# Performance work log

Hardware: AMD Instinct MI355X
Metric: run time of the kernel (lower is better)

Reference implementation:

```python
import jax, jax.numpy as jnp
import numpy as np

# Dimensions (TinyLlama-like)
B, T = 4, 1024
D = 2048          # hidden_size
H, DH = 32, 64    # heads, head_dim
HK = 8            # kv heads (GQA, n_rep = 4)
RQ, RKV = 32, 32  # per-head SVD ranks
RO, RF = 1024, 1024
I = 5632          # intermediate_size
THETA = 10000.0
EPS = 1e-5


def setup_inputs() -> dict:
    key = jax.random.key(0)
    ks = jax.random.split(key, 16)
    p = lambda k, s: jax.random.normal(k, s, jnp.float32) * 0.02
    return {
        "x": jax.random.normal(ks[0], (B, T, D), jnp.float32),
        "ln1_w": jnp.ones((D,), jnp.float32),
        "ln2_w": jnp.ones((D,), jnp.float32),
        "q_Us": p(ks[1], (H, DH, RQ)),  "q_V": p(ks[2], (H, RQ, D)),
        "k_Us": p(ks[3], (HK, DH, RKV)), "k_V": p(ks[4], (HK, RKV, D)),
        "v_Us": p(ks[5], (HK, DH, RKV)), "v_V": p(ks[6], (HK, RKV, D)),
        "o_Us": p(ks[7], (D, RO)),  "o_V": p(ks[8], (RO, H * DH)),
        "g_Us": p(ks[9], (I, RF)),  "g_V": p(ks[10], (RF, D)),
        "u_Us": p(ks[11], (I, RF)), "u_V": p(ks[12], (RF, D)),
        "d_Us": p(ks[13], (D, RF)), "d_V": p(ks[14], (RF, I)),
    }


def _rms(x, w):
    return x * jax.lax.rsqrt(jnp.mean(x * x, axis=-1, keepdims=True) + EPS) * w


def _rope_cos_sin(t_len, dh, dtype):
    half = dh // 2
    inv_freq = 1.0 / (THETA ** (jnp.arange(half, dtype=jnp.float32) / half))
    ang = jnp.arange(t_len, dtype=jnp.float32)[:, None] * inv_freq[None, :]  # [T, half]
    return jnp.cos(ang).astype(dtype), jnp.sin(ang).astype(dtype)


def _apply_rope(x, cos, sin):
    # x: [B,h,T,Dh], LLaMA half-split rotation
    half = x.shape[-1] // 2
    x1, x2 = x[..., :half], x[..., half:]
    c = cos[None, None]  # [1,1,T,half]
    s = sin[None, None]
    return jnp.concatenate([x1 * c - x2 * s, x2 * c + x1 * s], axis=-1)


def reference(x, ln1_w, ln2_w, q_Us, q_V, k_Us, k_V, v_Us, v_V,
              o_Us, o_V, g_Us, g_V, u_Us, u_V, d_Us, d_V):
    b, t, d = x.shape
    h1 = _rms(x, ln1_w)

    # per-head low-rank projections: y_h = x @ V_h^T @ Us_h^T
    q = jnp.einsum('bhtr,hdr->bhtd', jnp.einsum('btD,hrD->bhtr', h1, q_V), q_Us)  # [B,H,T,Dh]
    k = jnp.einsum('bhtr,hdr->bhtd', jnp.einsum('btD,hrD->bhtr', h1, k_V), k_Us)  # [B,Hk,T,Dh]
    v = jnp.einsum('bhtr,hdr->bhtd', jnp.einsum('btD,hrD->bhtr', h1, v_V), v_Us)

    cos, sin = _rope_cos_sin(t, DH, x.dtype)
    q = _apply_rope(q, cos, sin)
    k = _apply_rope(k, cos, sin)

    n_rep = H // HK
    k = jnp.repeat(k, n_rep, axis=1)  # _repeat_kv
    v = jnp.repeat(v, n_rep, axis=1)

    scale = 1.0 / np.sqrt(DH)
    scores = jnp.einsum('bhtd,bhsd->bhts', q, k) * scale
    causal = jnp.tril(jnp.ones((t, t), bool))
    scores = jnp.where(causal[None, None], scores, jnp.finfo(scores.dtype).min)
    attn = jax.nn.softmax(scores, axis=-1)
    ctx = jnp.einsum('bhts,bhsd->bhtd', attn, v)
    ctx = ctx.transpose(0, 2, 1, 3).reshape(b, t, H * DH)

    # low-rank output proj: o = ctx @ o_V^T @ o_Us^T
    attn_out = jnp.einsum('btr,Dr->btD', jnp.einsum('btk,rk->btr', ctx, o_V), o_Us)
    x = x + attn_out

    # SwiGLU MLP with low-rank factors
    h2 = _rms(x, ln2_w)
    g = jnp.einsum('btr,ir->bti', jnp.einsum('btD,rD->btr', h2, g_V), g_Us)
    u = jnp.einsum('btr,ir->bti', jnp.einsum('btD,rD->btr', h2, u_V), u_Us)
    ff = jax.nn.silu(g) * u
    down = jnp.einsum('btr,Dr->btD', jnp.einsum('bti,ri->btr', ff, d_V), d_Us)
    return x + down
```

## Files before the change

kernel.cpp:

```cpp
#include <hip/hip_runtime.h>
#include <math.h>

typedef unsigned short u16;
typedef unsigned int u32;
typedef __bf16 bf16x8 __attribute__((ext_vector_type(8)));
typedef float f32x4 __attribute__((ext_vector_type(4)));

__device__ __forceinline__ float bf2f(u16 u) {
  union { u32 i; float f; } x; x.i = ((u32)u) << 16; return x.f;
}
__device__ __forceinline__ u16 f2bf(float f) {
  union { float f; u32 i; } x; x.f = f;
  return (u16)((x.i + 0x7fffu + ((x.i >> 16) & 1u)) >> 16);
}

#define GLDS16(gp, lp)                                                        \
  __builtin_amdgcn_global_load_lds(                                           \
      (const __attribute__((address_space(1))) u32*)(gp),                     \
      (__attribute__((address_space(3))) u32*)(lp), 16, 0, 0)

__global__ void detect_k(const u16* __restrict__ w, int* __restrict__ flag) {
  if (threadIdx.x == 0 && blockIdx.x == 0)
    *flag = (w[0] == 0x0000u && w[1] == 0x3F80u) ? 1 : 0;
}

__global__ __launch_bounds__(256) void rope_tab_k(float2* __restrict__ tab) {
  const int idx = blockIdx.x * 256 + threadIdx.x;
  const int t = idx >> 5, j = idx & 31;
  float inv = powf(10000.0f, -(float)j * (1.0f / 32.0f));
  float ang = (float)t * inv;
  float sn, cs;
  sincosf(ang, &sn, &cs);
  tab[idx] = make_float2(cs, sn);
}

struct CvtArgs {
  const void* src[17];
  u32 dstOff[17];
  u32 blkOff[18];
};

__global__ __launch_bounds__(256) void cvt_all(CvtArgs a, u16* __restrict__ dstB,
                                               const int* __restrict__ flag,
                                               const void* __restrict__ w1src,
                                               u16* __restrict__ h1) {
  int seg = 0;
  const int bx = blockIdx.x;
#pragma unroll 1
  while (bx >= (int)a.blkOff[seg + 1]) seg++;
  const int tid = threadIdx.x;
  const long local = ((long)(bx - a.blkOff[seg]) * 256 + tid) * 8;
  u16* dst = dstB + a.dstOff[seg] + local;
  const bool f32in = (*flag != 0);
  uint4 o; u16* op = (u16*)&o;
  if (f32in) {
    const float* s = (const float*)a.src[seg] + local;
    float4 va = *(const float4*)(s);
    float4 vb = *(const float4*)(s + 4);
    op[0] = f2bf(va.x); op[1] = f2bf(va.y); op[2] = f2bf(va.z); op[3] = f2bf(va.w);
    op[4] = f2bf(vb.x); op[5] = f2bf(vb.y); op[6] = f2bf(vb.z); op[7] = f2bf(vb.w);
  } else {
    o = *(const uint4*)((const u16*)a.src[seg] + local);
  }
  *(uint4*)dst = o;

  if (seg == 0) {
    float v[8];
    float ss = 0.f;
#pragma unroll
    for (int i = 0; i < 8; i++) { v[i] = bf2f(op[i]); ss += v[i] * v[i]; }
#pragma unroll
    for (int off = 32; off > 0; off >>= 1) ss += __shfl_xor(ss, off);
    __shared__ float red[4];
    if ((tid & 63) == 0) red[tid >> 6] = ss;
    __syncthreads();
    const float total = red[0] + red[1] + red[2] + red[3];
    const float inv = rsqrtf(total * (1.0f / 2048.0f) + 1e-5f);
    float wv[8];
    if (f32in) {
      const float* wp = (const float*)w1src + tid * 8;
      float4 wa = *(const float4*)(wp);
      float4 wb = *(const float4*)(wp + 4);
      wv[0] = bf2f(f2bf(wa.x)); wv[1] = bf2f(f2bf(wa.y));
      wv[2] = bf2f(f2bf(wa.z)); wv[3] = bf2f(f2bf(wa.w));
      wv[4] = bf2f(f2bf(wb.x)); wv[5] = bf2f(f2bf(wb.y));
      wv[6] = bf2f(f2bf(wb.z)); wv[7] = bf2f(f2bf(wb.w));
    } else {
      uint4 ww = *((const uint4*)w1src + tid);
      const u16* wp = (const u16*)&ww;
#pragma unroll
      for (int i = 0; i < 8; i++) wv[i] = bf2f(wp[i]);
    }
    uint4 ho; u16* hop = (u16*)&ho;
#pragma unroll
    for (int i = 0; i < 8; i++) hop[i] = f2bf(v[i] * inv * wv[i]);
    *(uint4*)(h1 + (long)bx * 2048 + tid * 8) = ho;
  }
}

__global__ __launch_bounds__(256) void rms_k(const u16* __restrict__ x,
                                             const u16* __restrict__ w,
                                             u16* __restrict__ out) {
  const long row = blockIdx.x;
  const u16* xr = x + row * 2048;
  u16* orow = out + row * 2048;
  const int tid = threadIdx.x;
  const int base = tid * 8;
  uint4 u = *(const uint4*)(xr + base);
  const u16* us = (const u16*)&u;
  float v[8];
  float ss = 0.f;
#pragma unroll
  for (int i = 0; i < 8; i++) { v[i] = bf2f(us[i]); ss += v[i] * v[i]; }
#pragma unroll
  for (int off = 32; off > 0; off >>= 1) ss += __shfl_xor(ss, off);
  __shared__ float red[4];
  if ((tid & 63) == 0) red[tid >> 6] = ss;
  __syncthreads();
  float total = red[0] + red[1] + red[2] + red[3];
  float inv = rsqrtf(total * (1.0f / 2048.0f) + 1e-5f);
  uint4 wv = *(const uint4*)(w + base);
  const u16* wp = (const u16*)&wv;
  uint4 o;
  u16* op = (u16*)&o;
#pragma unroll
  for (int i = 0; i < 8; i++) op[i] = f2bf(v[i] * inv * bf2f(wp[i]));
  *(uint4*)(orow + base) = o;
}

template <int EPI>
__global__ __launch_bounds__(256, 3) void gemm_bt(const u16* __restrict__ A,
                                                  const u16* __restrict__ B,
                                                  void* Cv,
                                                  void* Cv2,
                                                  const u16* R,
                                                  const int* flagp,
                                                  int N, int Klen, int lda, int ldb) {
  __shared__ u16 As[128 * 32];
  __shared__ u16 Bs[128 * 32];
  const long koff = (long)blockIdx.z * Klen;
  A += koff;
  B += koff;
  if (blockIdx.z) Cv = Cv2;
  const int m0 = blockIdx.y * 128;
  const int n0 = blockIdx.x * 128;
  const int tid = threadIdx.x;
  const int wave = tid >> 6;
  const int lane = tid & 63;
  const int wr = (wave >> 1) * 64;
  const int wc = (wave & 1) * 64;
  const int l16 = lane & 15;
  const int quad = lane >> 4;
  u16* C = (u16*)Cv;
  float* Cf = (float*)Cv;
  bool f32o = false;
  if (EPI == 3) f32o = (*flagp != 0);

  f32x4 acc[4][4];
#pragma unroll
  for (int i = 0; i < 4; i++)
#pragma unroll
    for (int j = 0; j < 4; j++) acc[i][j] = (f32x4){0.f, 0.f, 0.f, 0.f};

  const int srow = wave * 16 + (lane >> 2);
  const int scol = (lane & 3) * 8;
  const u16* Ag = A + (long)(m0 + srow) * lda + scol;
  const u16* Bg = B + (long)(n0 + srow) * ldb + scol;
  const long astep = (long)64 * lda;
  const long bstep = (long)64 * ldb;
  u16* Asw = &As[wave * 16 * 32];
  u16* Bsw = &Bs[wave * 16 * 32];

  for (int k0 = 0; k0 < Klen; k0 += 32) {
    GLDS16(Ag + k0, Asw);
    GLDS16(Ag + astep + k0, Asw + 64 * 32);
    GLDS16(Bg + k0, Bsw);
    GLDS16(Bg + bstep + k0, Bsw + 64 * 32);
    __syncthreads();
    bf16x8 af[4], bfr[4];
#pragma unroll
    for (int t = 0; t < 4; t++) {
      af[t]  = *(const bf16x8*)(&As[(wr + t * 16 + l16) * 32 + quad * 8]);
      bfr[t] = *(const bf16x8*)(&Bs[(wc + t * 16 + l16) * 32 + quad * 8]);
    }
#pragma unroll
    for (int i = 0; i < 4; i++)
#pragma unroll
      for (int j = 0; j < 4; j++)
        acc[i][j] = __builtin_amdgcn_mfma_f32_16x16x32_bf16(bfr[j], af[i], acc[i][j], 0, 0, 0);
    __syncthreads();
  }

#pragma unroll
  for (int i = 0; i < 4; i++) {
    const int m = m0 + wr + i * 16 + l16;
#pragma unroll
    for (int j = 0; j < 4; j++) {
      const int n = n0 + wc + j * 16 + quad * 4;
      const long idx = (long)m * N + n;
      float v[4];
#pragma unroll
      for (int r = 0; r < 4; r++) v[r] = acc[i][j][r];
      if (EPI == 1 || EPI == 3) {
        uint2 rr = *(const uint2*)(R + idx);
        const u16* rp = (const u16*)&rr;
#pragma unroll
        for (int r = 0; r < 4; r++) v[r] += bf2f(rp[r]);
      }
      if (EPI == 3 && f32o) {
        float4 o = {v[0], v[1], v[2], v[3]};
        *(float4*)(Cf + idx) = o;
      } else {
        uint2 o; u16* op = (u16*)&o;
#pragma unroll
        for (int r = 0; r < 4; r++) op[r] = f2bf(v[r]);
        *(uint2*)(C + idx) = o;
      }
    }
  }
}

#define STAGE_SILU(buf, k0)                                                   \
  do {                                                                        \
    GLDS16(Ag_ + (k0), &SH[buf][0][woff]);                                    \
    GLDS16(Au_ + (k0), &SH[buf][1][woff]);                                    \
    GLDS16(Bg_ + (k0), &SH[buf][2][woff]);                                    \
    GLDS16(Bu_ + (k0), &SH[buf][3][woff]);                                    \
  } while (0)

__global__ __launch_bounds__(512, 4) void gemm_silu(const u16* __restrict__ Agp,
                                                    const u16* __restrict__ Aup,
                                                    const u16* __restrict__ Bgp,
                                                    const u16* __restrict__ Bup,
                                                    u16* __restrict__ C,
                                                    int N, int Klen, int lda, int ldb) {
  __shared__ u16 SH[2][4][128 * 32];
  const int m0 = blockIdx.y * 128;
  const int n0 = blockIdx.x * 128;
  const int tid = threadIdx.x;
  const int wave = tid >> 6;
  const int lane = tid & 63;
  const int wid = wave & 3;
  const int isU = wave >> 2;
  const int wr = (wid >> 1) * 64;
  const int wc = (wid & 1) * 64;
  const int l16 = lane & 15;
  const int quad = lane >> 4;
  const int matA = isU;
  const int matB = 2 + isU;

  f32x4 acc[4][4];
#pragma unroll
  for (int i = 0; i < 4; i++)
#pragma unroll
    for (int j = 0; j < 4; j++) acc[i][j] = (f32x4){0.f, 0.f, 0.f, 0.f};

  const int srow = wave * 16 + (lane >> 2);
  const int scol = ((lane & 3) ^ ((lane >> 3) & 3)) * 8;
  const u16* Ag_ = Agp + (long)(m0 + srow) * lda + scol;
  const u16* Au_ = Aup + (long)(m0 + srow) * lda + scol;
  const u16* Bg_ = Bgp + (long)(n0 + srow) * ldb + scol;
  const u16* Bu_ = Bup + (long)(n0 + srow) * ldb + scol;
  const int woff = wave * 512;
  const int rsw = (quad ^ ((l16 >> 1) & 3)) * 8;

  const int nk = Klen >> 5;
  STAGE_SILU(0, 0);
  int cur = 0;
  for (int kt = 0; kt < nk; ++kt) {
    if (kt + 1 < nk) {
      STAGE_SILU(cur ^ 1, (kt + 1) << 5);
      asm volatile("s_waitcnt vmcnt(4)" ::: "memory");
    } else {
      asm volatile("s_waitcnt vmcnt(0)" ::: "memory");
    }
    asm volatile("s_barrier" ::: "memory");
    bf16x8 af[4], bfr[4];
#pragma unroll
    for (int t = 0; t < 4; t++) {
      af[t]  = *(const bf16x8*)(&SH[cur][matA][(wr + t * 16 + l16) * 32 + rsw]);
      bfr[t] = *(const bf16x8*)(&SH[cur][matB][(wc + t * 16 + l16) * 32 + rsw]);
    }
#pragma unroll
    for (int i = 0; i < 4; i++)
#pragma unroll
      for (int j = 0; j < 4; j++)
        acc[i][j] = __builtin_amdgcn_mfma_f32_16x16x32_bf16(bfr[j], af[i], acc[i][j], 0, 0, 0);
    asm volatile("s_barrier" ::: "memory");
    cur ^= 1;
  }

  float* xch = (float*)&SH[0][0][0];
  if (isU) {
    float* w = xch + wid * 4096 + lane * 4;
#pragma unroll
    for (int i = 0; i < 4; i++)
#pragma unroll
      for (int j = 0; j < 4; j++)
        *(f32x4*)(w + (i * 4 + j) * 256) = acc[i][j];
  }
  __syncthreads();
  if (!isU) {
    const float* w = xch + wid * 4096 + lane * 4;
#pragma unroll
    for (int i = 0; i < 4; i++) {
      const int m = m0 + wr + i * 16 + l16;
#pragma unroll
      for (int j = 0; j < 4; j++) {
        const int n = n0 + wc + j * 16 + quad * 4;
        const long idx = (long)m * N + n;
        f32x4 uv = *(const f32x4*)(w + (i * 4 + j) * 256);
        uint2 o; u16* op = (u16*)&o;
#pragma unroll
        for (int r = 0; r < 4; r++) {
          float g = acc[i][j][r];
          float v = uv[r] * g / (1.f + __expf(-g));
          op[r] = f2bf(v);
        }
        *(uint2*)(C + idx) = o;
      }
    }
  }
}

__global__ __launch_bounds__(256) void combine2(const u16* __restrict__ a,
                                                const u16* __restrict__ b,
                                                u16* __restrict__ o) {
  const long i = ((long)blockIdx.x * 256 + threadIdx.x) * 8;
  uint4 ua = *(const uint4*)(a + i);
  uint4 ub = *(const uint4*)(b + i);
  const u16* pa = (const u16*)&ua;
  const u16* pb = (const u16*)&ub;
  uint4 uo; u16* po = (u16*)&uo;
#pragma unroll
  for (int j = 0; j < 8; j++) po[j] = f2bf(bf2f(pa[j]) + bf2f(pb[j]));
  *(uint4*)(o + i) = uo;
}

__global__ __launch_bounds__(256) void expand_fused(const u16* __restrict__ p0,
                                                    const u16* __restrict__ p1,
                                                    const u16* __restrict__ qUs,
                                                    const u16* __restrict__ kUs,
                                                    const u16* __restrict__ vUs,
                                                    u16* __restrict__ qout,
                                                    u16* __restrict__ kout,
                                                    u16* __restrict__ vout,
                                                    const float2* __restrict__ tab) {
  const int tok = blockIdx.x;
  const int wave = threadIdx.x >> 6;
  const int d = threadIdx.x & 63;
  const int y = blockIdx.y;
  int mode, hbase;
  if (y < 8)       { mode = 0; hbase = y * 4; }
  else if (y < 10) { mode = 1; hbase = (y - 8) * 4; }
  else             { mode = 2; hbase = (y - 10) * 4; }
  const int h = hbase + wave;
  const int b = tok >> 10;
  const int t = tok & 1023;
  const int roff = (mode == 0) ? 0 : (mode == 1 ? 1024 : 1280);
  const u16* Us = (mode == 0) ? qUs : (mode == 1 ? kUs : vUs);
  const u16* up = Us + ((long)h * 64 + d) * 32;
  const long rbase = (long)tok * 1536 + roff + h * 32;
  const u16* rp0 = p0 + rbase;
  const u16* rp1 = p1 + rbase;
  float s = 0.f;
#pragma unroll
  for (int c = 0; c < 4; c++) {
    uint4 uu = *(const uint4*)(up + c * 8);
    uint4 r0 = *(const uint4*)(rp0 + c * 8);
    uint4 r1 = *(const uint4*)(rp1 + c * 8);
    const u16* u8p = (const u16*)&uu;
    const u16* r0p = (const u16*)&r0;
    const u16* r1p = (const u16*)&r1;
#pragma unroll
    for (int i = 0; i < 8; i++) s += bf2f(u8p[i]) * (bf2f(r0p[i]) + bf2f(r1p[i]));
  }
  if (mode < 2) {
    const int j = d & 31;
    float2 cs2 = tab[(t << 5) | j];
    float partner = __shfl_xor(s, 32);
    s = (d < 32) ? (s * cs2.x - partner * cs2.y) : (s * cs2.x + partner * cs2.y);
  }
  const u16 val = f2bf(s);
  if (mode == 0)      qout[(((long)(b * 32 + h)) * 1024 + t) * 64 + d] = val;
  else if (mode == 1) kout[(((long)(b * 8 + h)) * 1024 + t) * 64 + d] = val;
  else                vout[(((long)(b * 8 + h)) * 1024 + t) * 64 + d] = val;
}

__global__ __launch_bounds__(256) void vT_k(const u16* __restrict__ vbuf,
                                            u16* __restrict__ vT) {
  __shared__ u16 tile[64][72];
  const int b = blockIdx.z, kh = blockIdx.y;
  const int t0 = blockIdx.x * 64;
  const int tid = threadIdx.x;
  const int r = tid >> 2;
  const int c = (tid & 3) * 16;
  const u16* src = vbuf + ((long)(b * 8 + kh) * 1024 + t0 + r) * 64 + c;
  *(uint4*)&tile[r][c] = *(const uint4*)src;
  *(uint4*)&tile[r][c + 8] = *(const uint4*)(src + 8);
  __syncthreads();
  u16 tmp[16];
#pragma unroll
  for (int i = 0; i < 16; i++) tmp[i] = tile[c + i][r];
  u16* dst = vT + ((long)(b * 8 + kh) * 64 + r) * 1024 + t0 + c;
  *(uint4*)dst = *(uint4*)&tmp[0];
  *(uint4*)(dst + 8) = *(uint4*)&tmp[8];
}

#define ATS 72

__global__ __launch_bounds__(256, 2) void attn_mfma(const u16* __restrict__ q,
                                                    const u16* __restrict__ k,
                                                    const u16* __restrict__ vT,
                                                    u16* __restrict__ ctx) {
  __shared__ u16 Ks[64 * ATS];
  __shared__ u16 Vts[64 * ATS];
  __shared__ u16 Plds[4][16 * ATS];
  const int bx = blockIdx.x;
  const int h = blockIdx.y;
  const int b = blockIdx.z;
  const int kh = h >> 2;
  const int qlo = bx * 64;
  const int qhi = (15 - bx) * 64;
  const int tid = threadIdx.x;
  const int wave = tid >> 6;
  const int lane = tid & 63;
  const int l16 = lane & 15;
  const int quad = lane >> 4;

  const u16* qb = q + ((long)(b * 32 + h) * 1024) * 64;
  const u16* kb = k + ((long)(b * 8 + kh) * 1024) * 64;
  const u16* vb = vT + ((long)(b * 8 + kh) * 64) * 1024;

  bf16x8 qfl[2], qfh[2];
  {
    const u16* qp = qb + (long)(qlo + wave * 16 + l16) * 64 + quad * 8;
    qfl[0] = *(const bf16x8*)(qp);
    qfl[1] = *(const bf16x8*)(qp + 32);
    qp = qb + (long)(qhi + wave * 16 + l16) * 64 + quad * 8;
    qfh[0] = *(const bf16x8*)(qp);
    qfh[1] = *(const bf16x8*)(qp + 32);
  }

  float ml[4], ll[4], mh[4], lh[4];
  f32x4 ol[4], oh[4];
#pragma unroll
  for (int r = 0; r < 4; r++) { ml[r] = -1e30f; ll[r] = 0.f; mh[r] = -1e30f; lh[r] = 0.f; }
#pragma unroll
  for (int j = 0; j < 4; j++) { ol[j] = (f32x4){0.f, 0.f, 0.f, 0.f}; oh[j] = ol[j]; }

  const int srow = tid >> 2;
  const int sc0 = (tid & 3) * 16;
  int s0 = 0;

  auto process = [&](const bf16x8* qf, float* m, float* l, f32x4* oacc, int qtb) {
    f32x4 s[4];
    __builtin_amdgcn_s_setprio(1);
#pragma unroll
    for (int t = 0; t < 4; t++) {
      s[t] = (f32x4){0.f, 0.f, 0.f, 0.f};
      const u16* kr = &Ks[(t * 16 + l16) * ATS + quad * 8];
      bf16x8 b0 = *(const bf16x8*)(kr);
      bf16x8 b1 = *(const bf16x8*)(kr + 32);
      s[t] = __builtin_amdgcn_mfma_f32_16x16x32_bf16(qf[0], b0, s[t], 0, 0, 0);
      s[t] = __builtin_amdgcn_mfma_f32_16x16x32_bf16(qf[1], b1, s[t], 0, 0, 0);
    }
    __builtin_amdgcn_s_setprio(0);
#pragma unroll
    for (int t = 0; t < 4; t++) s[t] *= 0.125f;
    if (s0 == qtb) {
#pragma unroll
      for (int t = 0; t < 4; t++)
#pragma unroll
        for (int r = 0; r < 4; r++)
          if (s0 + t * 16 + l16 > qtb + wave * 16 + quad * 4 + r) s[t][r] = -1e30f;
    }
    float p[4][4];
#pragma unroll
    for (int r = 0; r < 4; r++) {
      float mx = fmaxf(fmaxf(s[0][r], s[1][r]), fmaxf(s[2][r], s[3][r]));
#pragma unroll
      for (int off = 1; off < 16; off <<= 1) mx = fmaxf(mx, __shfl_xor(mx, off));
      const float mnew = fmaxf(m[r], mx);
      const float alpha = __expf(m[r] - mnew);
      float ps = 0.f;
#pragma unroll
      for (int t = 0; t < 4; t++) { p[t][r] = __expf(s[t][r] - mnew); ps += p[t][r]; }
#pragma unroll
      for (int off = 1; off < 16; off <<= 1) ps += __shfl_xor(ps, off);
      l[r] = l[r] * alpha + ps;
      m[r] = mnew;
#pragma unroll
      for (int j = 0; j < 4; j++) oacc[j][r] *= alpha;
    }
    u16* pw = &Plds[wave][0];
#pragma unroll
    for (int t = 0; t < 4; t++)
#pragma unroll
      for (int r = 0; r < 4; r++)
        pw[(quad * 4 + r) * ATS + t * 16 + l16] = f2bf(p[t][r]);
    bf16x8 pf0 = *(const bf16x8*)(&pw[l16 * ATS + quad * 8]);
    bf16x8 pf1 = *(const bf16x8*)(&pw[l16 * ATS + 32 + quad * 8]);
    __builtin_amdgcn_s_setprio(1);
#pragma unroll
    for (int j = 0; j < 4; j++) {
      const u16* vr = &Vts[(j * 16 + l16) * ATS + quad * 8];
      bf16x8 v0 = *(const bf16x8*)(vr);
      bf16x8 v1 = *(const bf16x8*)(vr + 32);
      oacc[j] = __builtin_amdgcn_mfma_f32_16x16x32_bf16(pf0, v0, oacc[j], 0, 0, 0);
      oacc[j] = __builtin_amdgcn_mfma_f32_16x16x32_bf16(pf1, v1, oacc[j], 0, 0, 0);
    }
    __builtin_amdgcn_s_setprio(0);
  };

  uint4 kA, kB, vA, vB;
  {
    const u16* kp = kb + (long)srow * 64 + sc0;
    kA = *(const uint4*)kp;
    kB = *(const uint4*)(kp + 8);
    const u16* vp = vb + (long)srow * 1024 + sc0;
    vA = *(const uint4*)vp;
    vB = *(const uint4*)(vp + 8);
  }

  for (s0 = 0; s0 <= qhi; s0 += 64) {
    __syncthreads();
    *(uint4*)&Ks[srow * ATS + sc0] = kA;
    *(uint4*)&Ks[srow * ATS + sc0 + 8] = kB;
    *(uint4*)&Vts[srow * ATS + sc0] = vA;
    *(uint4*)&Vts[srow * ATS + sc0 + 8] = vB;
    __syncthreads();
    if (s0 + 64 <= qhi) {
      const u16* kp = kb + (long)(s0 + 64 + srow) * 64 + sc0;
      kA = *(const uint4*)kp;
      kB = *(const uint4*)(kp + 8);
      const u16* vp = vb + (long)srow * 1024 + (s0 + 64) + sc0;
      vA = *(const uint4*)vp;
      vB = *(const uint4*)(vp + 8);
    }
    process(qfh, mh, lh, oh, qhi);
    if (s0 <= qlo) process(qfl, ml, ll, ol, qlo);
  }

#pragma unroll
  for (int r = 0; r < 4; r++) {
    const int rowl = qlo + wave * 16 + quad * 4 + r;
    const int rowh = qhi + wave * 16 + quad * 4 + r;
    const float il = 1.f / ll[r];
    const float ih = 1.f / lh[r];
#pragma unroll
    for (int j = 0; j < 4; j++) {
      ctx[(((long)(b * 1024 + rowl)) * 32 + h) * 64 + j * 16 + l16] = f2bf(ol[j][r] * il);
      ctx[(((long)(b * 1024 + rowh)) * 32 + h) * 64 + j * 16 + l16] = f2bf(oh[j][r] * ih);
    }
  }
}

extern "C" void kernel_launch(void* const* d_in, const int* in_sizes, int n_in,
                              void* d_out, int out_size, void* d_ws, size_t ws_size,
                              hipStream_t stream) {
  char* ws = (char*)d_ws;
  u16* cb = (u16*)ws;
  u16* cx    = cb + 0;
  u16* cln2  = cb + 8390656;
  u16* cqUs  = cb + 8392704;
  u16* ckUs  = cb + 8458240;
  u16* cvUs  = cb + 8474624;
  u16* cqkvV = cb + 8491008;
  u16* coUs  = cb + 11636736;
  u16* coV   = cb + 13733888;
  u16* cguV  = cb + 15831040;
  u16* cgUs  = cb + 20025344;
  u16* cuUs  = cb + 25792512;
  u16* cdUs  = cb + 31559680;
  u16* cdV   = cb + 33656832;

  char* P = ws + 78848000;
  u16* h1    = (u16*)(P + 0);
  u16* kbuf  = (u16*)(P + 0);
  u16* vbuf  = (u16*)(P + 4194304);
  u16* qbuf  = (u16*)(P + 16777216);
  u16* qp0   = (u16*)(P + 33554432);
  u16* qp1   = (u16*)(P + 46137344);
  u16* ctx   = (u16*)(P + 58720256);
  u16* vbufT = (u16*)(P + 75497472);
  u16* orr   = (u16*)(P + 75497472);
  u16* xmid  = (u16*)(P + 83886080);
  u16* op0   = (u16*)(P + 0);
  u16* op1   = (u16*)(P + 8388608);
  u16* h2    = (u16*)(P + 0);
  u16* gur   = (u16*)(P + 16777216);
  u16* gbuf  = (u16*)(P + 33554432);
  u16* dp0   = (u16*)(P + 0);
  u16* dp1   = (u16*)(P + 8388608);
  u16* dr    = (u16*)(P + 16777216);
  float2* ropetab = (float2*)(P + 79691776);
  int* flag  = (int*)(ws + 179511296);

  const dim3 blk(256);
  detect_k<<<1, 64, 0, stream>>>((const u16*)d_in[1], flag);
  rope_tab_k<<<128, blk, 0, stream>>>(ropetab);

  CvtArgs ca;
  const u32 dOff[17] = {0u, 8388608u, 8390656u, 8392704u, 8491008u, 8458240u,
                        10588160u, 8474624u, 11112448u, 11636736u, 13733888u,
                        20025344u, 15831040u, 25792512u, 17928192u, 31559680u,
                        33656832u};
  const u32 nblk[17] = {4096u, 1u, 1u, 32u, 1024u, 8u, 256u, 8u, 256u, 1024u,
                        1024u, 2816u, 1024u, 2816u, 1024u, 1024u, 2816u};
  u32 cum = 0;
  for (int i = 0; i < 17; i++) {
    ca.src[i] = d_in[i];
    ca.dstOff[i] = dOff[i];
    ca.blkOff[i] = cum;
    cum += nblk[i];
  }
  ca.blkOff[17] = cum;
  cvt_all<<<cum, blk, 0, stream>>>(ca, cb, flag, d_in[1], h1);

  gemm_bt<0><<<dim3(12, 32, 2), blk, 0, stream>>>(h1, cqkvV, qp0, qp1, nullptr, nullptr, 1536, 1024, 2048, 2048);
  expand_fused<<<dim3(4096, 12), blk, 0, stream>>>(qp0, qp1, cqUs, ckUs, cvUs,
                                                   qbuf, kbuf, vbuf, ropetab);
  vT_k<<<dim3(16, 8, 4), blk, 0, stream>>>(vbuf, vbufT);
  attn_mfma<<<dim3(8, 32, 4), blk, 0, stream>>>(qbuf, kbuf, vbufT, ctx);
  gemm_bt<0><<<dim3(8, 32, 2), blk, 0, stream>>>(ctx, coV, op0, op1, nullptr, nullptr, 1024, 1024, 2048, 2048);
  combine2<<<2048, blk, 0, stream>>>(op0, op1, orr);
  gemm_bt<1><<<dim3(16, 32), blk, 0, stream>>>(orr, coUs, xmid, nullptr, cx, nullptr, 2048, 1024, 1024, 1024);
  rms_k<<<4096, blk, 0, stream>>>(xmid, cln2, h2);
  gemm_bt<0><<<dim3(16, 32), blk, 0, stream>>>(h2, cguV, gur, nullptr, nullptr, nullptr, 2048, 2048, 2048, 2048);
  gemm_silu<<<dim3(44, 32), dim3(512), 0, stream>>>(gur, gur + 1024, cgUs, cuUs, gbuf, 5632, 1024, 2048, 1024);
  gemm_bt<0><<<dim3(8, 32, 2), blk, 0, stream>>>(gbuf, cdV, dp0, dp1, nullptr, nullptr, 1024, 2816, 5632, 5632);
  combine2<<<2048, blk, 0, stream>>>(dp0, dp1, dr);
  gemm_bt<3><<<dim3(16, 32), blk, 0, stream>>>(dr, cdUs, d_out, nullptr, xmid, flag, 2048, 1024, 1024, 1024);
}
```

Before: 762.7 us.

## Increase split-K across GEMMs and move residual epilogues into combine kernels

Removes the templated epilogue from gemm_bt so it always writes bf16 partials at a strided offset per K-split. The ctx and down V-projections now split K four ways, and the O-Us, gate/up-V and down-Us GEMMs split two ways. New combine4 and combine_res kernels sum the partials, with combine_res also adding the residual and selecting the fp32 output. This raises block counts to fill more CUs, at the cost of extra partial-buffer traffic, extra launches and rounding each partial to bf16.

After: 795.9 us. 4.3% more time.

```diff
diff --git a/kernel.cpp b/kernel.cpp
--- a/kernel.cpp
+++ b/kernel.cpp
@@ -128,20 +128,17 @@
   *(uint4*)(orow + base) = o;
 }
 
-template <int EPI>
 __global__ __launch_bounds__(256, 3) void gemm_bt(const u16* __restrict__ A,
                                                   const u16* __restrict__ B,
-                                                  void* Cv,
-                                                  void* Cv2,
-                                                  const u16* R,
-                                                  const int* flagp,
+                                                  u16* __restrict__ C,
+                                                  long cstride,
                                                   int N, int Klen, int lda, int ldb) {
   __shared__ u16 As[128 * 32];
   __shared__ u16 Bs[128 * 32];
   const long koff = (long)blockIdx.z * Klen;
   A += koff;
   B += koff;
-  if (blockIdx.z) Cv = Cv2;
+  C = (u16*)((char*)C + (long)blockIdx.z * cstride);
   const int m0 = blockIdx.y * 128;
   const int n0 = blockIdx.x * 128;
   const int tid = threadIdx.x;
@@ -151,10 +148,6 @@
   const int wc = (wave & 1) * 64;
   const int l16 = lane & 15;
   const int quad = lane >> 4;
-  u16* C = (u16*)Cv;
-  float* Cf = (float*)Cv;
-  bool f32o = false;
-  if (EPI == 3) f32o = (*flagp != 0);
 
   f32x4 acc[4][4];
 #pragma unroll
@@ -198,24 +191,10 @@
     for (int j = 0; j < 4; j++) {
       const int n = n0 + wc + j * 16 + quad * 4;
       const long idx = (long)m * N + n;
-      float v[4];
-#pragma unroll
-      for (int r = 0; r < 4; r++) v[r] = acc[i][j][r];
-      if (EPI == 1 || EPI == 3) {
-        uint2 rr = *(const uint2*)(R + idx);
-        const u16* rp = (const u16*)&rr;
-#pragma unroll
-        for (int r = 0; r < 4; r++) v[r] += bf2f(rp[r]);
-      }
-      if (EPI == 3 && f32o) {
-        float4 o = {v[0], v[1], v[2], v[3]};
-        *(float4*)(Cf + idx) = o;
-      } else {
-        uint2 o; u16* op = (u16*)&o;
-#pragma unroll
-        for (int r = 0; r < 4; r++) op[r] = f2bf(v[r]);
-        *(uint2*)(C + idx) = o;
-      }
+      uint2 o; u16* op = (u16*)&o;
+#pragma unroll
+      for (int r = 0; r < 4; r++) op[r] = f2bf(acc[i][j][r]);
+      *(uint2*)(C + idx) = o;
     }
   }
 }
@@ -335,6 +314,56 @@
 #pragma unroll
   for (int j = 0; j < 8; j++) po[j] = f2bf(bf2f(pa[j]) + bf2f(pb[j]));
   *(uint4*)(o + i) = uo;
+}
+
+__global__ __launch_bounds__(256) void combine4(const u16* __restrict__ a,
+                                                const u16* __restrict__ b,
+                                                const u16* __restrict__ c,
+                                                const u16* d,
+                                                u16* o) {
+  const long i = ((long)blockIdx.x * 256 + threadIdx.x) * 8;
+  uint4 ua = *(const uint4*)(a + i);
+  uint4 ub = *(const uint4*)(b + i);
+  uint4 uc = *(const uint4*)(c + i);
+  uint4 ud = *(const uint4*)(d + i);
+  const u16* pa = (const u16*)&ua;
+  const u16* pb = (const u16*)&ub;
+  const u16* pc = (const u16*)&uc;
+  const u16* pd = (const u16*)&ud;
+  uint4 uo; u16* po = (u16*)&uo;
+#pragma unroll
+  for (int j = 0; j < 8; j++)
+    po[j] = f2bf((bf2f(pa[j]) + bf2f(pb[j])) + (bf2f(pc[j]) + bf2f(pd[j])));
+  *(uint4*)(o + i) = uo;
+}
+
+template <int FIN>
+__global__ __launch_bounds__(256) void combine_res(const u16* __restrict__ a,
+                                                   const u16* __restrict__ b,
+                                                   const u16* __restrict__ r,
+                                                   void* __restrict__ ov,
+                                                   const int* flagp) {
+  const long i = ((long)blockIdx.x * 256 + threadIdx.x) * 8;
+  uint4 ua = *(const uint4*)(a + i);
+  uint4 ub = *(const uint4*)(b + i);
+  uint4 ur = *(const uint4*)(r + i);
+  const u16* pa = (const u16*)&ua;
+  const u16* pb = (const u16*)&ub;
+  const u16* pr = (const u16*)&ur;
+  float v[8];
+#pragma unroll
+  for (int j = 0; j < 8; j++) v[j] = bf2f(pa[j]) + bf2f(pb[j]) + bf2f(pr[j]);
+  if (FIN == 1 && *flagp) {
+    float4 o0 = {v[0], v[1], v[2], v[3]};
+    float4 o1 = {v[4], v[5], v[6], v[7]};
+    *(float4*)((float*)ov + i) = o0;
+    *(float4*)((float*)ov + i + 4) = o1;
+  } else {
+    uint4 uo; u16* po = (u16*)&uo;
+#pragma unroll
+    for (int j = 0; j < 8; j++) po[j] = f2bf(v[j]);
+    *(uint4*)((u16*)ov + i) = uo;
+  }
 }
 
 __global__ __launch_bounds__(256) void expand_fused(const u16* __restrict__ p0,
@@ -588,12 +617,22 @@
   u16* xmid  = (u16*)(P + 83886080);
   u16* op0   = (u16*)(P + 0);
   u16* op1   = (u16*)(P + 8388608);
+  u16* op2   = (u16*)(P + 16777216);
+  u16* op3   = (u16*)(P + 25165824);
+  u16* up0   = (u16*)(P + 0);
+  u16* up1   = (u16*)(P + 16777216);
   u16* h2    = (u16*)(P + 0);
+  u16* gu0   = (u16*)(P + 33554432);
+  u16* gu1   = (u16*)(P + 50331648);
   u16* gur   = (u16*)(P + 16777216);
   u16* gbuf  = (u16*)(P + 33554432);
   u16* dp0   = (u16*)(P + 0);
   u16* dp1   = (u16*)(P + 8388608);
-  u16* dr    = (u16*)(P + 16777216);
+  u16* dp2   = (u16*)(P + 16777216);
+  u16* dp3   = (u16*)(P + 25165824);
+  u16* dr    = dp3;
+  u16* f0    = (u16*)(P + 33554432);
+  u16* f1    = (u16*)(P + 50331648);
   float2* ropetab = (float2*)(P + 79691776);
   int* flag  = (int*)(ws + 179511296);
 
@@ -618,18 +657,21 @@
   ca.blkOff[17] = cum;
   cvt_all<<<cum, blk, 0, stream>>>(ca, cb, flag, d_in[1], h1);
 
-  gemm_bt<0><<<dim3(12, 32, 2), blk, 0, stream>>>(h1, cqkvV, qp0, qp1, nullptr, nullptr, 1536, 1024, 2048, 2048);
+  gemm_bt<<<dim3(12, 32, 2), blk, 0, stream>>>(h1, cqkvV, qp0, 12582912L, 1536, 1024, 2048, 2048);
   expand_fused<<<dim3(4096, 12), blk, 0, stream>>>(qp0, qp1, cqUs, ckUs, cvUs,
                                                    qbuf, kbuf, vbuf, ropetab);
   vT_k<<<dim3(16, 8, 4), blk, 0, stream>>>(vbuf, vbufT);
   attn_mfma<<<dim3(8, 32, 4), blk, 0, stream>>>(qbuf, kbuf, vbufT, ctx);
-  gemm_bt<0><<<dim3(8, 32, 2), blk, 0, stream>>>(ctx, coV, op0, op1, nullptr, nullptr, 1024, 1024, 2048, 2048);
-  combine2<<<2048, blk, 0, stream>>>(op0, op1, orr);
-  gemm_bt<1><<<dim3(16, 32), blk, 0, stream>>>(orr, coUs, xmid, nullptr, cx, nullptr, 2048, 1024, 1024, 1024);
+  gemm_bt<<<dim3(8, 32, 4), blk, 0, stream>>>(ctx, coV, op0, 8388608L, 1024, 512, 2048, 2048);
+  combine4<<<2048, blk, 0, stream>>>(op0, op1, op2, op3, orr);
+  gemm_bt<<<dim3(16, 32, 2), blk, 0, stream>>>(orr, coUs, up0, 16777216L, 2048, 512, 1024, 1024);
+  combine_res<0><<<4096, blk, 0, stream>>>(up0, up1, cx, xmid, nullptr);
   rms_k<<<4096, blk, 0, stream>>>(xmid, cln2, h2);
-  gemm_bt<0><<<dim3(16, 32), blk, 0, stream>>>(h2, cguV, gur, nullptr, nullptr, nullptr, 2048, 2048, 2048, 2048);
+  gemm_bt<<<dim3(16, 32, 2), blk, 0, stream>>>(h2, cguV, gu0, 16777216L, 2048, 1024, 2048, 2048);
+  combine2<<<4096, blk, 0, stream>>>(gu0, gu1, gur);
   gemm_silu<<<dim3(44, 32), dim3(512), 0, stream>>>(gur, gur + 1024, cgUs, cuUs, gbuf, 5632, 1024, 2048, 1024);
-  gemm_bt<0><<<dim3(8, 32, 2), blk, 0, stream>>>(gbuf, cdV, dp0, dp1, nullptr, nullptr, 1024, 2816, 5632, 5632);
-  combine2<<<2048, blk, 0, stream>>>(dp0, dp1, dr);
-  gemm_bt<3><<<dim3(16, 32), blk, 0, stream>>>(dr, cdUs, d_out, nullptr, xmid, flag, 2048, 1024, 1024, 1024);
-}
+  gemm_bt<<<dim3(8, 32, 4), blk, 0, stream>>>(gbuf, cdV, dp0, 8388608L, 1024, 1408, 5632, 5632);
+  combine4<<<2048, blk, 0, stream>>>(dp0, dp1, dp2, dp3, dr);
+  gemm_bt<<<dim3(16, 32, 2), blk, 0, stream>>>(dr, cdUs, f0, 16777216L, 2048, 512, 1024, 1024);
+  combine_res<1><<<4096, blk, 0, stream>>>(f0, f1, xmid, d_out, flag);
+}
```
